# Kernel tuning notes

Measured on AMD Instinct MI355X. Metric: run time of the kernel, lower is better.

The kernel has to match this reference:

```python
import jax, jax.numpy as jnp
import numpy as np

FG_FRACTION = 0.5
BATCHSIZE = 256
NUM_IMAGES = 1
NUM_CLASSES = 21
FG_THRESH = 0.5
BG_THRESH_HI = 0.5
BG_THRESH_LO = 0.1
ROIS_PER_IMAGE = BATCHSIZE // NUM_IMAGES                      # 256
FG_ROIS_PER_IMAGE = int(round(FG_FRACTION * ROIS_PER_IMAGE))  # 128
BG_ROIS_PER_IMAGE = ROIS_PER_IMAGE - FG_ROIS_PER_IMAGE        # 128


def _make_boxes(key, n, img=1000.0, max_wh=200.0):
    k1, k2 = jax.random.split(key)
    xy = jax.random.uniform(k1, (n, 2), dtype=jnp.float32) * (img - max_wh)
    wh = jax.random.uniform(k2, (n, 2), dtype=jnp.float32) * max_wh + 1.0
    return jnp.concatenate([xy, xy + wh], axis=1)  # valid [x1,y1,x2,y2]


def setup_inputs() -> dict:
    key = jax.random.key(0)
    k1, k2, k3 = jax.random.split(key, 3)
    N, G = 250000, 128
    rois = _make_boxes(k1, N)
    all_rois = jnp.concatenate([jnp.zeros((N, 1), jnp.float32), rois], axis=1)  # [N,5], col0 = image idx
    gt_boxes = _make_boxes(k2, G)                                               # [G,4]
    gt_labels = jax.random.randint(k3, (G,), 1, NUM_CLASSES).astype(jnp.int32)  # fg classes 1..20
    return {"all_rois": all_rois, "gt_boxes": gt_boxes, "gt_labels": gt_labels}


def _iou(a, b):
    area_a = (a[:, 2] - a[:, 0] + 1.0) * (a[:, 3] - a[:, 1] + 1.0)
    area_b = (b[:, 2] - b[:, 0] + 1.0) * (b[:, 3] - b[:, 1] + 1.0)
    ix1 = jnp.maximum(a[:, None, 0], b[None, :, 0])
    iy1 = jnp.maximum(a[:, None, 1], b[None, :, 1])
    ix2 = jnp.minimum(a[:, None, 2], b[None, :, 2])
    iy2 = jnp.minimum(a[:, None, 3], b[None, :, 3])
    iw = jnp.clip(ix2 - ix1 + 1.0, 0.0)
    ih = jnp.clip(iy2 - iy1 + 1.0, 0.0)
    inter = iw * ih
    return inter / (area_a[:, None] + area_b[None, :] - inter)


def _bbox_transform(ex, gt):
    ew = ex[:, 2] - ex[:, 0] + 1.0
    eh = ex[:, 3] - ex[:, 1] + 1.0
    ecx = ex[:, 0] + 0.5 * ew
    ecy = ex[:, 1] + 0.5 * eh
    gw = gt[:, 2] - gt[:, 0] + 1.0
    gh = gt[:, 3] - gt[:, 1] + 1.0
    gcx = gt[:, 0] + 0.5 * gw
    gcy = gt[:, 1] + 0.5 * gh
    return jnp.stack([(gcx - ecx) / ew, (gcy - ecy) / eh,
                      jnp.log(gw / ew), jnp.log(gh / eh)], axis=1)


def _proposal_target(all_rois, gt_boxes, gt_labels):
    G = gt_boxes.shape[0]
    # append gt boxes (with image-index 0 column) to the proposal set
    gt_rois = jnp.concatenate([jnp.zeros((G, 1), all_rois.dtype), gt_boxes], axis=1)
    all_rois = jnp.concatenate([all_rois, gt_rois], axis=0)          # [N+G, 5]

    overlaps = _iou(all_rois[:, 1:5], gt_boxes)                       # [N+G, G] -- dominant memory traffic
    gt_assignment = jnp.argmax(overlaps, axis=1)                      # [N+G]
    max_ov = jnp.max(overlaps, axis=1)                                # [N+G]
    labels_all = gt_labels[gt_assignment]                             # [N+G]

    fg_mask = max_ov >= FG_THRESH
    bg_mask = (max_ov < BG_THRESH_HI) & (max_ov >= BG_THRESH_LO)

    # random fg/bg sampling: top-k over random keys restricted to each mask
    u = jax.random.uniform(jax.random.key(42), (all_rois.shape[0],), dtype=jnp.float32)
    fg_idx = jax.lax.top_k(jnp.where(fg_mask, u, -1.0), FG_ROIS_PER_IMAGE)[1]
    bg_idx = jax.lax.top_k(jnp.where(bg_mask, u, -1.0), BG_ROIS_PER_IMAGE)[1]
    keep = jnp.concatenate([fg_idx, bg_idx])                          # [256]

    valid_fg = fg_mask[fg_idx]  # if fewer fg than requested, pad slots get label 0
    labels = jnp.concatenate([jnp.where(valid_fg, labels_all[fg_idx], 0),
                              jnp.zeros((BG_ROIS_PER_IMAGE,), labels_all.dtype)])

    rois = all_rois[keep]                                             # [256, 5]
    targets = _bbox_transform(rois[:, 1:5], gt_boxes[gt_assignment[keep]])  # [256, 4]

    # scatter targets into class-specific columns [256, 4*num_classes]
    onehot = jax.nn.one_hot(labels, NUM_CLASSES, dtype=targets.dtype)
    bbox_targets = (onehot[:, :, None] * targets[:, None, :]).reshape(ROIS_PER_IMAGE, 4 * NUM_CLASSES)
    bbox_targets = bbox_targets * (labels > 0)[:, None].astype(targets.dtype)
    return rois, labels, bbox_targets


def reference(all_rois, gt_boxes, gt_labels):
    return _proposal_target(all_rois, gt_boxes, gt_labels)
```

## Files before the change

kernel.cpp:

```cpp
#include <hip/hip_runtime.h>
#include <stdint.h>

#define GMAX 128
#define TK 128
#define NBINS 4096
#define CAND_MAX 4096
#define NUM_CLASSES 21
#define CBLOCK 1024
#define CBLOCKS 62

__device__ __forceinline__ void threefry2x32(uint32_t k0, uint32_t k1,
                                             uint32_t& x0, uint32_t& x1) {
  uint32_t ks0 = k0, ks1 = k1, ks2 = k0 ^ k1 ^ 0x1BD11BDAu;
  x0 += ks0; x1 += ks1;
#define TF_ROUND(r) { x0 += x1; x1 = (x1 << (r)) | (x1 >> (32 - (r))); x1 ^= x0; }
  TF_ROUND(13) TF_ROUND(15) TF_ROUND(26) TF_ROUND(6)
  x0 += ks1; x1 += ks2 + 1u;
  TF_ROUND(17) TF_ROUND(29) TF_ROUND(16) TF_ROUND(24)
  x0 += ks2; x1 += ks0 + 2u;
  TF_ROUND(13) TF_ROUND(15) TF_ROUND(26) TF_ROUND(6)
  x0 += ks0; x1 += ks1 + 3u;
  TF_ROUND(17) TF_ROUND(29) TF_ROUND(16) TF_ROUND(24)
  x0 += ks1; x1 += ks2 + 4u;
  TF_ROUND(13) TF_ROUND(15) TF_ROUND(26) TF_ROUND(6)
  x0 += ks2; x1 += ks0 + 5u;
#undef TF_ROUND
}

__global__ void __launch_bounds__(256)
score_kernel(const float* __restrict__ all_rois,
             const float* __restrict__ gt_boxes,
             uint32_t* __restrict__ score,
             uint32_t* __restrict__ hist,
             int N, int M, int G) {
  __shared__ float sgx1[GMAX], sgy1[GMAX], sgx2[GMAX], sgy2[GMAX], sga[GMAX];
  const int t = threadIdx.x;
  if (t < G) {
    float x1 = gt_boxes[t * 4 + 0];
    float y1 = gt_boxes[t * 4 + 1];
    float x2 = gt_boxes[t * 4 + 2];
    float y2 = gt_boxes[t * 4 + 3];
    sgx1[t] = x1; sgy1[t] = y1; sgx2[t] = x2; sgy2[t] = y2;
    sga[t] = __fmul_rn(__fadd_rn(__fsub_rn(x2, x1), 1.0f),
                       __fadd_rn(__fsub_rn(y2, y1), 1.0f));
  }
  __syncthreads();
  const int i = blockIdx.x * 256 + t;
  if (i >= M) return;

  float bx1, by1, bx2, by2;
  if (i < N) {
    bx1 = all_rois[(size_t)i * 5 + 1];
    by1 = all_rois[(size_t)i * 5 + 2];
    bx2 = all_rois[(size_t)i * 5 + 3];
    by2 = all_rois[(size_t)i * 5 + 4];
  } else {
    int g = i - N;
    bx1 = sgx1[g]; by1 = sgy1[g]; bx2 = sgx2[g]; by2 = sgy2[g];
  }
  const float area = __fmul_rn(__fadd_rn(__fsub_rn(bx2, bx1), 1.0f),
                               __fadd_rn(__fsub_rn(by2, by1), 1.0f));
  float best = -1.0f;
  int bi = 0;
  for (int g = 0; g < G; ++g) {
    float ix1 = fmaxf(bx1, sgx1[g]);
    float iy1 = fmaxf(by1, sgy1[g]);
    float ix2 = fminf(bx2, sgx2[g]);
    float iy2 = fminf(by2, sgy2[g]);
    float iw = fmaxf(__fadd_rn(__fsub_rn(ix2, ix1), 1.0f), 0.0f);
    float ih = fmaxf(__fadd_rn(__fsub_rn(iy2, iy1), 1.0f), 0.0f);
    float inter = __fmul_rn(iw, ih);
    float uni = __fsub_rn(__fadd_rn(area, sga[g]), inter);
    float ov = __fdiv_rn(inter, uni);
    if (ov > best) { best = ov; bi = g; }
  }

  uint32_t cx0 = 0u, cx1 = (uint32_t)i;
  threefry2x32(0u, 42u, cx0, cx1);
  uint32_t ubits = (cx0 ^ cx1) >> 9;

  uint32_t fg = (best >= 0.5f) ? 1u : 0u;
  uint32_t bg = (!fg && best >= 0.1f) ? 1u : 0u;
  score[i] = (ubits << 9) | ((uint32_t)bi << 2) | (fg << 1) | bg;
  if (fg)      atomicAdd(&hist[ubits >> 11], 1u);
  else if (bg) atomicAdd(&hist[NBINS + (ubits >> 11)], 1u);
}

__global__ void __launch_bounds__(CBLOCK)
compact_kernel(const uint32_t* __restrict__ score, int M,
               const uint32_t* __restrict__ hist,
               int* __restrict__ meta_cnt,
               uint64_t* __restrict__ cand) {
  __shared__ uint64_t gs[CBLOCK];
  __shared__ int s_jstar[2], s_bth[2];
  const int t = threadIdx.x;

  {
    const int b0 = 4 * t;
    uint64_t acc = 0;
    for (int k = 0; k < 4; ++k)
      acc += ((uint64_t)hist[b0 + k] << 32) | (uint64_t)hist[NBINS + b0 + k];
    gs[t] = acc;
    if (t < 2) s_jstar[t] = -1;
    __syncthreads();
    for (int d = 1; d < CBLOCK; d <<= 1) {
      uint64_t add = (t + d < CBLOCK) ? gs[t + d] : 0ull;
      __syncthreads();
      gs[t] += add;
      __syncthreads();
    }
    uint32_t vfg = (uint32_t)(gs[t] >> 32);
    uint32_t vbg = (uint32_t)gs[t];
    uint32_t nfg = (t < CBLOCK - 1) ? (uint32_t)(gs[t + 1] >> 32) : 0u;
    uint32_t nbg = (t < CBLOCK - 1) ? (uint32_t)gs[t + 1] : 0u;
    if (vfg >= (uint32_t)TK && (t == CBLOCK - 1 || nfg < (uint32_t)TK)) s_jstar[0] = t;
    if (vbg >= (uint32_t)TK && (t == CBLOCK - 1 || nbg < (uint32_t)TK)) s_jstar[1] = t;
    __syncthreads();
    if (t == 0) {
      for (int m = 0; m < 2; ++m) {
        int j = s_jstar[m], B = -1;
        if (j >= 0) {
          uint32_t base = 0;
          if (j < CBLOCK - 1)
            base = (m == 0) ? (uint32_t)(gs[j + 1] >> 32) : (uint32_t)gs[j + 1];
          const uint32_t* h = hist + m * NBINS;
          B = 4 * j;
          for (int b = 4 * j + 3; b >= 4 * j; --b) {
            base += h[b];
            if (base >= (uint32_t)TK) { B = b; break; }
          }
        }
        s_bth[m] = B;
      }
    }
    __syncthreads();
  }

  for (int i = blockIdx.x * CBLOCK + t; i < M; i += CBLOCKS * CBLOCK) {
    uint32_t s = score[i];
    uint32_t mb = s & 3u;
    if (!mb) continue;
    int m = (mb & 2u) ? 0 : 1;
    int B = s_bth[m];
    if (B >= 0 && (int)(s >> 20) < B) continue;
    int p = atomicAdd(&meta_cnt[m], 1);
    if (p < CAND_MAX)
      cand[(size_t)m * CAND_MAX + p] =
          (((uint64_t)((s >> 9) + 1u)) << 32) | (uint64_t)(~(uint32_t)i);
  }
}

__global__ void __launch_bounds__(1024)
final_kernel(const float* __restrict__ all_rois,
             const float* __restrict__ gt_boxes,
             const int* __restrict__ gt_labels,
             const uint32_t* __restrict__ score,
             const uint64_t* __restrict__ cand_g,
             const int* __restrict__ meta_cnt,
             float* __restrict__ out, int N, int M) {
  __shared__ uint64_t cand[CAND_MAX];
  __shared__ int keep[2 * TK];
  __shared__ int fgvalid[TK];
  __shared__ float s_tx[2 * TK], s_ty[2 * TK], s_tw[2 * TK], s_th[2 * TK];
  __shared__ int s_label[2 * TK];
  const int t = threadIdx.x;

  for (int m = 0; m < 2; ++m) {
    int cnt = meta_cnt[m]; if (cnt > CAND_MAX) cnt = CAND_MAX;
    int P = TK;
    while (P < cnt) P <<= 1;
    for (int p = t; p < P; p += 1024)
      cand[p] = (p < cnt) ? cand_g[(size_t)m * CAND_MAX + p] : 0ull;
    __syncthreads();
    for (int k = 2; k <= P; k <<= 1) {
      for (int j = k >> 1; j > 0; j >>= 1) {
        for (int idx = t; idx < P; idx += 1024) {
          int l = idx ^ j;
          if (l > idx) {
            uint64_t a = cand[idx], b = cand[l];
            bool swp = ((idx & k) == 0) ? (a < b) : (a > b);
            if (swp) { cand[idx] = b; cand[l] = a; }
          }
        }
        __syncthreads();
      }
    }
    if (cnt < TK && t == 0) {
      int fill = cnt;
      uint32_t mask_bit = (m == 0) ? 2u : 1u;
      for (int i = 0; i < M && fill < TK; ++i)
        if (!(score[i] & mask_bit)) cand[fill++] = (uint64_t)(~(uint32_t)i);
    }
    __syncthreads();
    if (t < TK) {
      uint64_t c = cand[t];
      keep[m * TK + t] = (int)(~(uint32_t)(c & 0xFFFFFFFFull));
      if (m == 0) fgvalid[t] = ((c >> 32) != 0ull) ? 1 : 0;
    }
    __syncthreads();
  }

  const int R = 2 * TK;
  float* rois_out   = out;
  float* labels_out = out + (size_t)R * 5;
  float* bt_out     = out + (size_t)R * 5 + R;

  if (t < R) {
    const int i = keep[t];
    float rimg, rx1, ry1, rx2, ry2;
    if (i < N) {
      rimg = all_rois[(size_t)i * 5 + 0];
      rx1  = all_rois[(size_t)i * 5 + 1];
      ry1  = all_rois[(size_t)i * 5 + 2];
      rx2  = all_rois[(size_t)i * 5 + 3];
      ry2  = all_rois[(size_t)i * 5 + 4];
    } else {
      int g = i - N;
      rimg = 0.0f;
      rx1 = gt_boxes[g * 4 + 0]; ry1 = gt_boxes[g * 4 + 1];
      rx2 = gt_boxes[g * 4 + 2]; ry2 = gt_boxes[g * 4 + 3];
    }
    rois_out[t * 5 + 0] = rimg;
    rois_out[t * 5 + 1] = rx1;
    rois_out[t * 5 + 2] = ry1;
    rois_out[t * 5 + 3] = rx2;
    rois_out[t * 5 + 4] = ry2;

    const int ga = (int)((score[i] >> 2) & 127u);
    int label = (t < TK && fgvalid[t]) ? gt_labels[ga] : 0;
    labels_out[t] = (float)label;
    s_label[t] = label;

    float gx1 = gt_boxes[ga * 4 + 0], gy1 = gt_boxes[ga * 4 + 1];
    float gx2 = gt_boxes[ga * 4 + 2], gy2 = gt_boxes[ga * 4 + 3];
    float ew = rx2 - rx1 + 1.0f, eh = ry2 - ry1 + 1.0f;
    float ecx = rx1 + 0.5f * ew, ecy = ry1 + 0.5f * eh;
    float gw = gx2 - gx1 + 1.0f, gh = gy2 - gy1 + 1.0f;
    float gcx = gx1 + 0.5f * gw, gcy = gy1 + 0.5f * gh;
    s_tx[t] = (gcx - ecx) / ew;
    s_ty[t] = (gcy - ecy) / eh;
    s_tw[t] = logf(gw / ew);
    s_th[t] = logf(gh / eh);
  }
  __syncthreads();

  const int TOT = R * 4 * NUM_CLASSES;
  for (int idx = t; idx < TOT; idx += 1024) {
    int r = idx / (4 * NUM_CLASSES);
    int c = idx - r * (4 * NUM_CLASSES);
    int lab = s_label[r];
    float v = 0.0f;
    if (lab > 0 && (c >> 2) == lab) {
      int cc = c & 3;
      v = (cc == 0) ? s_tx[r] : (cc == 1) ? s_ty[r] : (cc == 2) ? s_tw[r] : s_th[r];
    }
    bt_out[idx] = v;
  }
}

extern "C" void kernel_launch(void* const* d_in, const int* in_sizes, int n_in,
                              void* d_out, int out_size, void* d_ws, size_t ws_size,
                              hipStream_t stream) {
  const float* all_rois = (const float*)d_in[0];
  const float* gt_boxes = (const float*)d_in[1];
  const int*   gt_labels = (const int*)d_in[2];
  const int N = in_sizes[0] / 5;
  const int G = in_sizes[2];
  const int M = N + G;

  char* ws = (char*)d_ws;
  int* meta = (int*)ws;
  uint32_t* hist = (uint32_t*)(ws + 256);
  size_t off = 256 + (size_t)2 * NBINS * 4;
  uint32_t* score = (uint32_t*)(ws + off);
  off += (((size_t)M * 4) + 255) & ~(size_t)255;
  uint64_t* cand = (uint64_t*)(ws + off);
  float* out = (float*)d_out;

  hipMemsetAsync(ws, 0, 256 + (size_t)2 * NBINS * 4, stream);
  score_kernel<<<(M + 255) / 256, 256, 0, stream>>>(all_rois, gt_boxes, score,
                                                    hist, N, M, G);
  compact_kernel<<<CBLOCKS, CBLOCK, 0, stream>>>(score, M, hist, meta, cand);
  final_kernel<<<1, 1024, 0, stream>>>(all_rois, gt_boxes, gt_labels, score,
                                       cand, meta, out, N, M);
}
```

Measured before the change: 116.8 us.

## Bin GT boxes into spatial grid and fuse compaction with final selection

Builds an 8x8 grid of 128-pixel cells in shared memory per block so each ROI tests IoU only against GT boxes overlapping its cells, instead of all 128. The compact and final kernels are merged into one launch, where the last block (detected with an atomic counter) does the sort and output. The threshold search uses wavefront shuffles and ballots in place of a block-wide shared-memory scan. Risks: every block now pays for building the grid, the grid assumes boxes lie within 0..1023, and the last-block pattern relies on fences being correct.

```diff
diff --git a/kernel.cpp b/kernel.cpp
--- a/kernel.cpp
+++ b/kernel.cpp
@@ -7,7 +7,6 @@
 #define CAND_MAX 4096
 #define NUM_CLASSES 21
 #define CBLOCK 1024
-#define CBLOCKS 62
 
 __device__ __forceinline__ void threefry2x32(uint32_t k0, uint32_t k1,
                                              uint32_t& x0, uint32_t& x1) {
@@ -34,7 +33,11 @@
              uint32_t* __restrict__ hist,
              int N, int M, int G) {
   __shared__ float sgx1[GMAX], sgy1[GMAX], sgx2[GMAX], sgy2[GMAX], sga[GMAX];
+  __shared__ int cnts[64];
+  __shared__ uint16_t cell_start[65];
+  __shared__ uint16_t entries[1216];
   const int t = threadIdx.x;
+
   if (t < G) {
     float x1 = gt_boxes[t * 4 + 0];
     float y1 = gt_boxes[t * 4 + 1];
@@ -44,7 +47,40 @@
     sga[t] = __fmul_rn(__fadd_rn(__fsub_rn(x2, x1), 1.0f),
                        __fadd_rn(__fsub_rn(y2, y1), 1.0f));
   }
-  __syncthreads();
+  if (t < 64) cnts[t] = 0;
+  __syncthreads();
+
+  int gcx0 = 0, gcx1 = 0, gcy0 = 0, gcy1 = 0;
+  if (t < G) {
+    gcx0 = min(max((int)sgx1[t] >> 7, 0), 7);
+    gcx1 = min(max((int)(sgx2[t] + 1.0f) >> 7, 0), 7);
+    gcy0 = min(max((int)sgy1[t] >> 7, 0), 7);
+    gcy1 = min(max((int)(sgy2[t] + 1.0f) >> 7, 0), 7);
+    for (int cy = gcy0; cy <= gcy1; ++cy)
+      for (int cx = gcx0; cx <= gcx1; ++cx)
+        atomicAdd(&cnts[cy * 8 + cx], 1);
+  }
+  __syncthreads();
+  if (t == 0) {
+    int acc = 0;
+    for (int k = 0; k < 64; ++k) {
+      cell_start[k] = (uint16_t)acc;
+      int c = cnts[k];
+      cnts[k] = acc;
+      acc += c;
+    }
+    cell_start[64] = (uint16_t)acc;
+  }
+  __syncthreads();
+  if (t < G) {
+    for (int cy = gcy0; cy <= gcy1; ++cy)
+      for (int cx = gcx0; cx <= gcx1; ++cx) {
+        int p = atomicAdd(&cnts[cy * 8 + cx], 1);
+        entries[p] = (uint16_t)t;
+      }
+  }
+  __syncthreads();
+
   const int i = blockIdx.x * 256 + t;
   if (i >= M) return;
 
@@ -60,104 +96,56 @@
   }
   const float area = __fmul_rn(__fadd_rn(__fsub_rn(bx2, bx1), 1.0f),
                                __fadd_rn(__fsub_rn(by2, by1), 1.0f));
+  const int bcx0 = min(max((int)bx1 >> 7, 0), 7);
+  const int bcx1 = min(max((int)(bx2 + 1.0f) >> 7, 0), 7);
+  const int bcy0 = min(max((int)by1 >> 7, 0), 7);
+  const int bcy1 = min(max((int)(by2 + 1.0f) >> 7, 0), 7);
+
   float best = -1.0f;
   int bi = 0;
-  for (int g = 0; g < G; ++g) {
-    float ix1 = fmaxf(bx1, sgx1[g]);
-    float iy1 = fmaxf(by1, sgy1[g]);
-    float ix2 = fminf(bx2, sgx2[g]);
-    float iy2 = fminf(by2, sgy2[g]);
-    float iw = fmaxf(__fadd_rn(__fsub_rn(ix2, ix1), 1.0f), 0.0f);
-    float ih = fmaxf(__fadd_rn(__fsub_rn(iy2, iy1), 1.0f), 0.0f);
-    float inter = __fmul_rn(iw, ih);
-    float uni = __fsub_rn(__fadd_rn(area, sga[g]), inter);
-    float ov = __fdiv_rn(inter, uni);
-    if (ov > best) { best = ov; bi = g; }
-  }
+  for (int cy = bcy0; cy <= bcy1; ++cy)
+    for (int cx = bcx0; cx <= bcx1; ++cx) {
+      const int c = cy * 8 + cx;
+      const int e0 = cell_start[c], e1 = cell_start[c + 1];
+      for (int e = e0; e < e1; ++e) {
+        const int g = entries[e];
+        float ix1 = fmaxf(bx1, sgx1[g]);
+        float iy1 = fmaxf(by1, sgy1[g]);
+        float ix2 = fminf(bx2, sgx2[g]);
+        float iy2 = fminf(by2, sgy2[g]);
+        float iw = fmaxf(__fadd_rn(__fsub_rn(ix2, ix1), 1.0f), 0.0f);
+        float ih = fmaxf(__fadd_rn(__fsub_rn(iy2, iy1), 1.0f), 0.0f);
+        float inter = __fmul_rn(iw, ih);
+        float uni = __fsub_rn(__fadd_rn(area, sga[g]), inter);
+        float ov = __fdiv_rn(inter, uni);
+        if (ov > best || (ov == best && g < bi)) { best = ov; bi = g; }
+      }
+    }
+  if (best <= 0.0f) bi = 0;
+  const float maxov = (best < 0.0f) ? 0.0f : best;
 
   uint32_t cx0 = 0u, cx1 = (uint32_t)i;
   threefry2x32(0u, 42u, cx0, cx1);
   uint32_t ubits = (cx0 ^ cx1) >> 9;
 
-  uint32_t fg = (best >= 0.5f) ? 1u : 0u;
-  uint32_t bg = (!fg && best >= 0.1f) ? 1u : 0u;
+  uint32_t fg = (maxov >= 0.5f) ? 1u : 0u;
+  uint32_t bg = (!fg && maxov >= 0.1f) ? 1u : 0u;
   score[i] = (ubits << 9) | ((uint32_t)bi << 2) | (fg << 1) | bg;
   if (fg)      atomicAdd(&hist[ubits >> 11], 1u);
   else if (bg) atomicAdd(&hist[NBINS + (ubits >> 11)], 1u);
 }
 
 __global__ void __launch_bounds__(CBLOCK)
-compact_kernel(const uint32_t* __restrict__ score, int M,
-               const uint32_t* __restrict__ hist,
-               int* __restrict__ meta_cnt,
-               uint64_t* __restrict__ cand) {
-  __shared__ uint64_t gs[CBLOCK];
-  __shared__ int s_jstar[2], s_bth[2];
-  const int t = threadIdx.x;
-
-  {
-    const int b0 = 4 * t;
-    uint64_t acc = 0;
-    for (int k = 0; k < 4; ++k)
-      acc += ((uint64_t)hist[b0 + k] << 32) | (uint64_t)hist[NBINS + b0 + k];
-    gs[t] = acc;
-    if (t < 2) s_jstar[t] = -1;
-    __syncthreads();
-    for (int d = 1; d < CBLOCK; d <<= 1) {
-      uint64_t add = (t + d < CBLOCK) ? gs[t + d] : 0ull;
-      __syncthreads();
-      gs[t] += add;
-      __syncthreads();
-    }
-    uint32_t vfg = (uint32_t)(gs[t] >> 32);
-    uint32_t vbg = (uint32_t)gs[t];
-    uint32_t nfg = (t < CBLOCK - 1) ? (uint32_t)(gs[t + 1] >> 32) : 0u;
-    uint32_t nbg = (t < CBLOCK - 1) ? (uint32_t)gs[t + 1] : 0u;
-    if (vfg >= (uint32_t)TK && (t == CBLOCK - 1 || nfg < (uint32_t)TK)) s_jstar[0] = t;
-    if (vbg >= (uint32_t)TK && (t == CBLOCK - 1 || nbg < (uint32_t)TK)) s_jstar[1] = t;
-    __syncthreads();
-    if (t == 0) {
-      for (int m = 0; m < 2; ++m) {
-        int j = s_jstar[m], B = -1;
-        if (j >= 0) {
-          uint32_t base = 0;
-          if (j < CBLOCK - 1)
-            base = (m == 0) ? (uint32_t)(gs[j + 1] >> 32) : (uint32_t)gs[j + 1];
-          const uint32_t* h = hist + m * NBINS;
-          B = 4 * j;
-          for (int b = 4 * j + 3; b >= 4 * j; --b) {
-            base += h[b];
-            if (base >= (uint32_t)TK) { B = b; break; }
-          }
-        }
-        s_bth[m] = B;
-      }
-    }
-    __syncthreads();
-  }
-
-  for (int i = blockIdx.x * CBLOCK + t; i < M; i += CBLOCKS * CBLOCK) {
-    uint32_t s = score[i];
-    uint32_t mb = s & 3u;
-    if (!mb) continue;
-    int m = (mb & 2u) ? 0 : 1;
-    int B = s_bth[m];
-    if (B >= 0 && (int)(s >> 20) < B) continue;
-    int p = atomicAdd(&meta_cnt[m], 1);
-    if (p < CAND_MAX)
-      cand[(size_t)m * CAND_MAX + p] =
-          (((uint64_t)((s >> 9) + 1u)) << 32) | (uint64_t)(~(uint32_t)i);
-  }
-}
-
-__global__ void __launch_bounds__(1024)
-final_kernel(const float* __restrict__ all_rois,
-             const float* __restrict__ gt_boxes,
-             const int* __restrict__ gt_labels,
-             const uint32_t* __restrict__ score,
-             const uint64_t* __restrict__ cand_g,
-             const int* __restrict__ meta_cnt,
-             float* __restrict__ out, int N, int M) {
+compact_final_kernel(const float* __restrict__ all_rois,
+                     const float* __restrict__ gt_boxes,
+                     const int* __restrict__ gt_labels,
+                     const uint32_t* __restrict__ score,
+                     const uint32_t* __restrict__ hist,
+                     int* __restrict__ meta,
+                     uint64_t* __restrict__ cand_g,
+                     float* __restrict__ out, int N, int M) {
+  __shared__ int s_bth[2];
+  __shared__ int s_last;
   __shared__ uint64_t cand[CAND_MAX];
   __shared__ int keep[2 * TK];
   __shared__ int fgvalid[TK];
@@ -165,16 +153,80 @@
   __shared__ int s_label[2 * TK];
   const int t = threadIdx.x;
 
+  if (t < 64) {
+    const int base = t << 6;
+    uint64_t csum = 0;
+    for (int k = 0; k < 64; ++k)
+      csum += ((uint64_t)hist[base + k] << 32) | (uint64_t)hist[NBINS + base + k];
+    uint64_t S = csum;
+#pragma unroll
+    for (int d = 1; d < 64; d <<= 1) {
+      uint64_t up = __shfl_down((unsigned long long)S, d, 64);
+      if (t + d < 64) S += up;
+    }
+    for (int m = 0; m < 2; ++m) {
+      uint32_t v = (m == 0) ? (uint32_t)(S >> 32) : (uint32_t)S;
+      uint64_t bm = __ballot(v >= (uint32_t)TK);
+      int B = -1;
+      if (bm != 0ull) {
+        int jl = 63 - __builtin_clzll(bm);
+        uint32_t basecnt = 0;
+        if (jl < 63) {
+          uint64_t Sn = __shfl((unsigned long long)S, jl + 1, 64);
+          basecnt = (m == 0) ? (uint32_t)(Sn >> 32) : (uint32_t)Sn;
+        }
+        uint32_t FS = hist[m * NBINS + (jl << 6) + t];
+#pragma unroll
+        for (int d = 1; d < 64; d <<= 1) {
+          uint32_t up = __shfl_down(FS, d, 64);
+          if (t + d < 64) FS += up;
+        }
+        FS += basecnt;
+        uint64_t bm2 = __ballot(FS >= (uint32_t)TK);
+        B = (jl << 6) + (63 - __builtin_clzll(bm2));
+      }
+      if (t == 0) s_bth[m] = B;
+    }
+  }
+  __syncthreads();
+
+  const int i = blockIdx.x * CBLOCK + t;
+  if (i < M) {
+    uint32_t s = score[i];
+    uint32_t mb = s & 3u;
+    if (mb) {
+      int m = (mb & 2u) ? 0 : 1;
+      int B = s_bth[m];
+      if (!(B >= 0 && (int)(s >> 20) < B)) {
+        int p = atomicAdd(&meta[m], 1);
+        if (p < CAND_MAX)
+          cand_g[(size_t)m * CAND_MAX + p] =
+              (((uint64_t)((s >> 9) + 1u)) << 32) | (uint64_t)(~(uint32_t)i);
+      }
+    }
+  }
+
+  __syncthreads();
+  __threadfence();
+  if (t == 0) {
+    int old = __hip_atomic_fetch_add(&meta[2], 1, __ATOMIC_ACQ_REL,
+                                     __HIP_MEMORY_SCOPE_AGENT);
+    s_last = (old == (int)gridDim.x - 1) ? 1 : 0;
+  }
+  __syncthreads();
+  if (!s_last) return;
+  __threadfence();
+
   for (int m = 0; m < 2; ++m) {
-    int cnt = meta_cnt[m]; if (cnt > CAND_MAX) cnt = CAND_MAX;
+    int cnt = meta[m]; if (cnt > CAND_MAX) cnt = CAND_MAX;
     int P = TK;
     while (P < cnt) P <<= 1;
-    for (int p = t; p < P; p += 1024)
+    for (int p = t; p < P; p += CBLOCK)
       cand[p] = (p < cnt) ? cand_g[(size_t)m * CAND_MAX + p] : 0ull;
     __syncthreads();
     for (int k = 2; k <= P; k <<= 1) {
       for (int j = k >> 1; j > 0; j >>= 1) {
-        for (int idx = t; idx < P; idx += 1024) {
+        for (int idx = t; idx < P; idx += CBLOCK) {
           int l = idx ^ j;
           if (l > idx) {
             uint64_t a = cand[idx], b = cand[l];
@@ -188,8 +240,8 @@
     if (cnt < TK && t == 0) {
       int fill = cnt;
       uint32_t mask_bit = (m == 0) ? 2u : 1u;
-      for (int i = 0; i < M && fill < TK; ++i)
-        if (!(score[i] & mask_bit)) cand[fill++] = (uint64_t)(~(uint32_t)i);
+      for (int ii = 0; ii < M && fill < TK; ++ii)
+        if (!(score[ii] & mask_bit)) cand[fill++] = (uint64_t)(~(uint32_t)ii);
     }
     __syncthreads();
     if (t < TK) {
@@ -206,16 +258,16 @@
   float* bt_out     = out + (size_t)R * 5 + R;
 
   if (t < R) {
-    const int i = keep[t];
+    const int ki = keep[t];
     float rimg, rx1, ry1, rx2, ry2;
-    if (i < N) {
-      rimg = all_rois[(size_t)i * 5 + 0];
-      rx1  = all_rois[(size_t)i * 5 + 1];
-      ry1  = all_rois[(size_t)i * 5 + 2];
-      rx2  = all_rois[(size_t)i * 5 + 3];
-      ry2  = all_rois[(size_t)i * 5 + 4];
+    if (ki < N) {
+      rimg = all_rois[(size_t)ki * 5 + 0];
+      rx1  = all_rois[(size_t)ki * 5 + 1];
+      ry1  = all_rois[(size_t)ki * 5 + 2];
+      rx2  = all_rois[(size_t)ki * 5 + 3];
+      ry2  = all_rois[(size_t)ki * 5 + 4];
     } else {
-      int g = i - N;
+      int g = ki - N;
       rimg = 0.0f;
       rx1 = gt_boxes[g * 4 + 0]; ry1 = gt_boxes[g * 4 + 1];
       rx2 = gt_boxes[g * 4 + 2]; ry2 = gt_boxes[g * 4 + 3];
@@ -226,7 +278,7 @@
     rois_out[t * 5 + 3] = rx2;
     rois_out[t * 5 + 4] = ry2;
 
-    const int ga = (int)((score[i] >> 2) & 127u);
+    const int ga = (int)((score[ki] >> 2) & 127u);
     int label = (t < TK && fgvalid[t]) ? gt_labels[ga] : 0;
     labels_out[t] = (float)label;
     s_label[t] = label;
@@ -245,7 +297,7 @@
   __syncthreads();
 
   const int TOT = R * 4 * NUM_CLASSES;
-  for (int idx = t; idx < TOT; idx += 1024) {
+  for (int idx = t; idx < TOT; idx += CBLOCK) {
     int r = idx / (4 * NUM_CLASSES);
     int c = idx - r * (4 * NUM_CLASSES);
     int lab = s_label[r];
@@ -280,7 +332,8 @@
   hipMemsetAsync(ws, 0, 256 + (size_t)2 * NBINS * 4, stream);
   score_kernel<<<(M + 255) / 256, 256, 0, stream>>>(all_rois, gt_boxes, score,
                                                     hist, N, M, G);
-  compact_kernel<<<CBLOCKS, CBLOCK, 0, stream>>>(score, M, hist, meta, cand);
-  final_kernel<<<1, 1024, 0, stream>>>(all_rois, gt_boxes, gt_labels, score,
-                                       cand, meta, out, N, M);
+  const int cblocks = (M + CBLOCK - 1) / CBLOCK;
+  compact_final_kernel<<<cblocks, CBLOCK, 0, stream>>>(all_rois, gt_boxes,
+                                                       gt_labels, score, hist,
+                                                       meta, cand, out, N, M);
 }
```

After: 190.7 us. 1.63x slower.
